# Kernel tuning notes

Measured on AMD Instinct MI355X. Metric: run time of the kernel, lower is better.

The kernel has to match this reference:

```python
import jax, jax.numpy as jnp
import numpy as np

N, E, H, L = 20000, 1_280_000, 64, 4


def setup_inputs() -> dict:
    key = jax.random.key(0)
    ks = jax.random.split(key, 24)
    inputs = jax.random.normal(ks[0], (1, N, 6), jnp.float32)
    node_masks = jnp.ones((1, N), jnp.int32)
    send_edges = jax.random.randint(ks[1], (E,), 0, N)
    recv_edges = jax.random.randint(ks[2], (E,), 0, N)

    def w(k, shape, scale=None):
        s = (1.0 / np.sqrt(shape[-2])) if scale is None else scale
        return (jax.random.normal(k, shape, jnp.float32) * s)

    d = dict(
        inputs=inputs, node_masks=node_masks,
        send_edges=send_edges, recv_edges=recv_edges,
        emb_w=w(ks[3], (1, H)), emb_b=jnp.zeros((H,), jnp.float32),
        edge_w1=w(ks[4], (L, 2 * H + 1, H)), edge_b1=jnp.zeros((L, H), jnp.float32),
        edge_w2=w(ks[5], (L, H, H)), edge_b2=jnp.zeros((L, H), jnp.float32),
        node_w1=w(ks[6], (L, 2 * H, H)), node_b1=jnp.zeros((L, H), jnp.float32),
        node_w2=w(ks[7], (L, H, H)), node_b2=jnp.zeros((L, H), jnp.float32),
        coord_w1=w(ks[8], (L, H, H)), coord_b1=jnp.zeros((L, H), jnp.float32),
        coord_wout=w(ks[9], (L, H, 1), scale=0.001),  # xavier gain=0.001, no bias
        vel_w1=w(ks[10], (L, H, H)), vel_b1=jnp.zeros((L, H), jnp.float32),
        vel_w2=w(ks[11], (L, H, 1)), vel_b2=jnp.zeros((L, 1), jnp.float32),
    )
    return d


def reference(inputs, node_masks, send_edges, recv_edges,
              emb_w, emb_b, edge_w1, edge_b1, edge_w2, edge_b2,
              node_w1, node_b1, node_w2, node_b2,
              coord_w1, coord_b1, coord_wout,
              vel_w1, vel_b1, vel_w2, vel_b2):
    silu = jax.nn.silu
    # node_masks is all-ones -> node_inds = arange(N); all nodes active.
    pos, vel = jnp.split(inputs, 2, axis=-1)          # [1,N,3] each
    h = jnp.linalg.norm(vel, axis=-1, keepdims=True)  # speed -> [1,N,1]
    h = h @ emb_w + emb_b                             # [1,N,H]
    coord = pos
    n = coord.shape[1]
    counts = jax.ops.segment_sum(jnp.ones_like(recv_edges, dtype=coord.dtype),
                                 recv_edges, num_segments=n)
    inv_cnt = (1.0 / jnp.maximum(counts, 1.0))[None, :, None]
    seg = lambda e: jax.ops.segment_sum(e, recv_edges, num_segments=n)

    for l in range(L):
        # coord2radial
        cd = coord[:, send_edges] - coord[:, recv_edges]        # [1,E,3]
        radial = jnp.sum(cd * cd, -1, keepdims=True)            # [1,E,1]
        # edge_model
        ef_in = jnp.concatenate([h[:, send_edges], h[:, recv_edges], radial], -1)
        ef = silu(silu(ef_in @ edge_w1[l] + edge_b1[l]) @ edge_w2[l] + edge_b2[l])
        # coord_model
        cm = silu(ef @ coord_w1[l] + coord_b1[l]) @ coord_wout[l]  # [1,E,1]
        trans = jnp.clip(cd * cm, -100.0, 100.0)
        agg_mean = jax.vmap(seg)(trans) * inv_cnt                  # scatter_mean
        # velocity update
        v_gate = silu(h @ vel_w1[l] + vel_b1[l]) @ vel_w2[l] + vel_b2[l]
        vel = agg_mean + v_gate * vel
        coord = coord + vel
        # node_model (recurrent residual)
        agg_sum = jax.vmap(seg)(ef)                                # scatter_sum
        hn = jnp.concatenate([h, agg_sum], -1)
        h = silu(hn @ node_w1[l] + node_b1[l]) @ node_w2[l] + node_b2[l] + h

    pred = jnp.concatenate([coord, vel], -1)  # [1,N,6] == pred_all (all active)
    return pred
```

## Files before the change

### kernel.cpp

```cpp
#include <hip/hip_runtime.h>
#include <math.h>

#define N_NODES 20000
#define N_EDGES 1280000
#define NLAYERS 4
#define NTILE (N_EDGES/32)
#define TSTRIDE 68
#define SCHUNK 79

typedef short bf16x8 __attribute__((ext_vector_type(8)));
typedef float f32x4  __attribute__((ext_vector_type(4)));
typedef long long i64;
typedef unsigned short us;

__device__ __forceinline__ float silu_f(float x) {
    return x / (1.0f + __expf(-x));
}

__device__ __forceinline__ us f2b(float x) {
    union { float f; unsigned u; } v; v.f = x;
    unsigned r = v.u + 0x7FFF + ((v.u >> 16) & 1);
    return (us)(r >> 16);
}
__device__ __forceinline__ float b2f(us u) {
    union { float f; unsigned u; } v; v.u = ((unsigned)u) << 16;
    return v.f;
}
__device__ __forceinline__ void split2r(float x, us& hi, us& lo) {
    hi = f2b(x);
    lo = f2b(x - b2f(hi));
}
__device__ __forceinline__ void split2f(float x, us& hi, us& lo) {
    union { float f; unsigned u; } v; v.f = x;
    hi = (us)(v.u >> 16);
    union { float f; unsigned u; } h; h.u = v.u & 0xFFFF0000u;
    union { float f; unsigned u; } r; r.f = x - h.f;
    lo = (us)(r.u >> 16);
}

__device__ __forceinline__ bf16x8 ld8(const us* p) {
    bf16x8 a;
    ((i64*)&a)[0] = *(const i64*)p;
    ((i64*)&a)[1] = *(const i64*)(p + 4);
    return a;
}

__device__ __forceinline__ void mfma3(f32x4& acc, bf16x8 ahi, bf16x8 alo,
                                      bf16x8 bhi, bf16x8 blo) {
    acc = __builtin_amdgcn_mfma_f32_16x16x32_bf16(ahi, bhi, acc, 0, 0, 0);
    acc = __builtin_amdgcn_mfma_f32_16x16x32_bf16(alo, bhi, acc, 0, 0, 0);
    acc = __builtin_amdgcn_mfma_f32_16x16x32_bf16(ahi, blo, acc, 0, 0, 0);
}

__global__ void k_init(const float* __restrict__ inp,
                       const float* __restrict__ emb_w,
                       const float* __restrict__ emb_b,
                       float* __restrict__ outv,
                       us* __restrict__ hbh, us* __restrict__ hbl) {
    int t = blockIdx.x * blockDim.x + threadIdx.x;
    int n = t >> 6, f = t & 63;
    if (n >= N_NODES) return;
    float vx = inp[n*6+3], vy = inp[n*6+4], vz = inp[n*6+5];
    float sp = sqrtf(vx*vx + vy*vy + vz*vz);
    float hv = sp * emb_w[f] + emb_b[f];
    us hi, lo; split2r(hv, hi, lo);
    hbh[t] = hi; hbl[t] = lo;
    if (f < 6) outv[n*6+f] = inp[n*6+f];
}

__global__ void k_cnt(const int* __restrict__ recv, int* __restrict__ counts) {
    int t = blockIdx.x*256 + threadIdx.x;
    if (t < N_EDGES) atomicAdd(&counts[recv[t]], 1);
}

__global__ void k_scan(const int* __restrict__ counts, int* __restrict__ rowstart,
                       int* __restrict__ cursor, int* __restrict__ tile2node) {
    __shared__ int buf[256];
    const int tid = threadIdx.x;
    const int lo = tid*SCHUNK;
    const int hi = (lo + SCHUNK < N_NODES) ? lo + SCHUNK : N_NODES;
    int s = 0;
    for (int i = lo; i < hi; ++i) s += counts[i];
    buf[tid] = s;
    __syncthreads();
    for (int off = 1; off < 256; off <<= 1) {
        int v = (tid >= off) ? buf[tid-off] : 0;
        __syncthreads();
        buf[tid] += v;
        __syncthreads();
    }
    int run = buf[tid] - s;
    for (int i = lo; i < hi; ++i) {
        rowstart[i] = run; cursor[i] = run;
        const int c = counts[i];
        for (int t = (run + 31) >> 5; t*32 < run + c; ++t) tile2node[t] = i;
        run += c;
    }
    if (tid < 20) rowstart[N_NODES + tid] = N_EDGES;
}

__global__ void k_scatter(const int* __restrict__ send, const int* __restrict__ recv,
                          int* __restrict__ cursor, us* __restrict__ sp16) {
    int t = blockIdx.x*256 + threadIdx.x;
    if (t < N_EDGES) {
        int p = atomicAdd(&cursor[recv[t]], 1);
        sp16[p] = (us)send[t];
    }
}

__global__ void k_prepw(const float* __restrict__ ew1, const float* __restrict__ ew2,
                        const float* __restrict__ cw1,
                        us* __restrict__ w1th, us* __restrict__ w1tl,
                        us* __restrict__ w2th, us* __restrict__ w2tl,
                        us* __restrict__ cw1th, us* __restrict__ cw1tl) {
    int t = blockIdx.x*256 + threadIdx.x;
    int l = t >> 14;
    int r = t & 16383;
    us hi, lo;
    if (r < 8192) {
        int n = r >> 7, k = r & 127;
        split2r(ew1[l*129*64 + k*64 + n], hi, lo);
        w1th[l*8192 + r] = hi; w1tl[l*8192 + r] = lo;
    } else if (r < 12288) {
        int rr = r - 8192; int n = rr >> 6, k = rr & 63;
        split2r(ew2[l*4096 + k*64 + n], hi, lo);
        w2th[l*4096 + n*64 + k] = hi; w2tl[l*4096 + n*64 + k] = lo;
    } else {
        int rr = r - 12288; int n = rr >> 6, k = rr & 63;
        split2r(cw1[l*4096 + k*64 + n], hi, lo);
        cw1th[l*4096 + n*64 + k] = hi; cw1tl[l*4096 + n*64 + k] = lo;
    }
}

__launch_bounds__(128, 4)
__global__ void k_edge(const us* __restrict__ sp16, const int* __restrict__ rowstart,
                       const int* __restrict__ tile2node,
                       const us* __restrict__ hbh, const us* __restrict__ hbl,
                       const float* __restrict__ outv,
                       const us* __restrict__ w1th, const us* __restrict__ w1tl,
                       const us* __restrict__ w2th, const us* __restrict__ w2tl,
                       const us* __restrict__ cw1th, const us* __restrict__ cw1tl,
                       const float* __restrict__ ew1, const float* __restrict__ eb1,
                       const float* __restrict__ eb2, const float* __restrict__ cb1,
                       const float* __restrict__ cwo,
                       float* __restrict__ aggs, float* __restrict__ aggm) {
    __shared__ us tileh[2][32*TSTRIDE];
    __shared__ us tilel[2][32*TSTRIDE];

    const int tid  = threadIdx.x;
    const int wid  = tid >> 6;
    const int lane = tid & 63;
    const int q    = lane >> 4;
    const int l15  = lane & 15;
    const int wbase = blockIdx.x*64 + wid*32;
    const int wtile = blockIdx.x*2 + wid;

    const int e0 = wbase + l15, e1 = e0 + 16;
    const int s0 = sp16[e0], s1 = sp16[e1];

    const int t2n = tile2node[wtile];
    const int wv = rowstart[t2n + 1 + l15];
    int seg0 = 0, seg1 = 0;
    #pragma unroll
    for (int i = 0; i < 16; ++i) {
        const int wi = __shfl(wv, i);
        seg0 += (e0 >= wi);
        seg1 += (e1 >= wi);
    }
    const int r0 = t2n + seg0, r1 = t2n + seg1;

    const float cdx0 = outv[s0*6+0]-outv[r0*6+0], cdy0 = outv[s0*6+1]-outv[r0*6+1], cdz0 = outv[s0*6+2]-outv[r0*6+2];
    const float cdx1 = outv[s1*6+0]-outv[r1*6+0], cdy1 = outv[s1*6+1]-outv[r1*6+1], cdz1 = outv[s1*6+2]-outv[r1*6+2];
    const float rad0 = cdx0*cdx0+cdy0*cdy0+cdz0*cdz0;
    const float rad1 = cdx1*cdx1+cdy1*cdy1+cdz1*cdz1;

    f32x4 acc[2][4];
    #pragma unroll
    for (int mu = 0; mu < 2; ++mu)
        #pragma unroll
        for (int t = 0; t < 4; ++t) acc[mu][t] = (f32x4){0.f,0.f,0.f,0.f};

    #pragma unroll
    for (int kc = 0; kc < 4; ++kc) {
        const int off = (kc & 1)*32 + q*8;
        const size_t o0 = (size_t)((kc < 2) ? s0 : r0)*64 + off;
        const size_t o1 = (size_t)((kc < 2) ? s1 : r1)*64 + off;
        bf16x8 a0h = ld8(hbh + o0), a0l = ld8(hbl + o0);
        bf16x8 a1h = ld8(hbh + o1), a1l = ld8(hbl + o1);
        #pragma unroll
        for (int t = 0; t < 4; ++t) {
            const int wo = (16*t + l15)*128 + kc*32 + q*8;
            bf16x8 bh = ld8(w1th + wo), bl = ld8(w1tl + wo);
            mfma3(acc[0][t], a0h, a0l, bh, bl);
            mfma3(acc[1][t], a1h, a1l, bh, bl);
        }
    }

    float rsh0[4], rsh1[4];
    #pragma unroll
    for (int r = 0; r < 4; ++r) {
        rsh0[r] = __shfl(rad0, 4*q + r);
        rsh1[r] = __shfl(rad1, 4*q + r);
    }
    #pragma unroll
    for (int t = 0; t < 4; ++t) {
        const int col = 16*t + l15;
        const float wl = ew1[128*64 + col];
        const float bb = eb1[col];
        #pragma unroll
        for (int r = 0; r < 4; ++r) {
            acc[0][t][r] += rsh0[r]*wl + bb;
            acc[1][t][r] += rsh1[r]*wl + bb;
        }
    }

    us* Th = tileh[wid];
    us* Tl = tilel[wid];
    #pragma unroll
    for (int mu = 0; mu < 2; ++mu)
        #pragma unroll
        for (int t = 0; t < 4; ++t)
            #pragma unroll
            for (int r = 0; r < 4; ++r) {
                us hi, lo; split2f(silu_f(acc[mu][t][r]), hi, lo);
                const int ti = (mu*16 + 4*q + r)*TSTRIDE + 16*t + l15;
                Th[ti] = hi; Tl[ti] = lo;
            }
    __asm__ volatile("s_waitcnt lgkmcnt(0)" ::: "memory");

    #pragma unroll
    for (int mu = 0; mu < 2; ++mu)
        #pragma unroll
        for (int t = 0; t < 4; ++t) acc[mu][t] = (f32x4){0.f,0.f,0.f,0.f};
    #pragma unroll
    for (int kc = 0; kc < 2; ++kc) {
        const int t0 = l15*TSTRIDE + kc*32 + q*8;
        const int t1i = (16+l15)*TSTRIDE + kc*32 + q*8;
        bf16x8 a0h = ld8(Th + t0),  a0l = ld8(Tl + t0);
        bf16x8 a1h = ld8(Th + t1i), a1l = ld8(Tl + t1i);
        #pragma unroll
        for (int t = 0; t < 4; ++t) {
            const int wo = (16*t + l15)*64 + kc*32 + q*8;
            bf16x8 bh = ld8(w2th + wo), bl = ld8(w2tl + wo);
            mfma3(acc[0][t], a0h, a0l, bh, bl);
            mfma3(acc[1][t], a1h, a1l, bh, bl);
        }
    }

    float ef[2][4][4];
    #pragma unroll
    for (int t = 0; t < 4; ++t) {
        const float bb = eb2[16*t + l15];
        #pragma unroll
        for (int mu = 0; mu < 2; ++mu)
            #pragma unroll
            for (int r = 0; r < 4; ++r)
                ef[mu][t][r] = silu_f(acc[mu][t][r] + bb);
    }
    __asm__ volatile("s_waitcnt lgkmcnt(0)" ::: "memory");
    #pragma unroll
    for (int mu = 0; mu < 2; ++mu)
        #pragma unroll
        for (int t = 0; t < 4; ++t)
            #pragma unroll
            for (int r = 0; r < 4; ++r) {
                us hi, lo; split2f(ef[mu][t][r], hi, lo);
                const int ti = (mu*16 + 4*q + r)*TSTRIDE + 16*t + l15;
                Th[ti] = hi; Tl[ti] = lo;
            }
    __asm__ volatile("s_waitcnt lgkmcnt(0)" ::: "memory");

    #pragma unroll
    for (int mu = 0; mu < 2; ++mu)
        #pragma unroll
        for (int t = 0; t < 4; ++t) acc[mu][t] = (f32x4){0.f,0.f,0.f,0.f};
    #pragma unroll
    for (int kc = 0; kc < 2; ++kc) {
        const int t0 = l15*TSTRIDE + kc*32 + q*8;
        const int t1i = (16+l15)*TSTRIDE + kc*32 + q*8;
        bf16x8 a0h = ld8(Th + t0),  a0l = ld8(Tl + t0);
        bf16x8 a1h = ld8(Th + t1i), a1l = ld8(Tl + t1i);
        #pragma unroll
        for (int t = 0; t < 4; ++t) {
            const int wo = (16*t + l15)*64 + kc*32 + q*8;
            bf16x8 bh = ld8(cw1th + wo), bl = ld8(cw1tl + wo);
            mfma3(acc[0][t], a0h, a0l, bh, bl);
            mfma3(acc[1][t], a1h, a1l, bh, bl);
        }
    }

    float cm0[4] = {0.f,0.f,0.f,0.f}, cm1[4] = {0.f,0.f,0.f,0.f};
    #pragma unroll
    for (int t = 0; t < 4; ++t) {
        const int col = 16*t + l15;
        const float cb = cb1[col];
        const float co = cwo[col];
        #pragma unroll
        for (int r = 0; r < 4; ++r) {
            cm0[r] += silu_f(acc[0][t][r] + cb) * co;
            cm1[r] += silu_f(acc[1][t][r] + cb) * co;
        }
    }
    #pragma unroll
    for (int m = 1; m <= 8; m <<= 1)
        #pragma unroll
        for (int r = 0; r < 4; ++r) {
            cm0[r] += __shfl_xor(cm0[r], m);
            cm1[r] += __shfl_xor(cm1[r], m);
        }

    int   sgrow[2][4];
    float tv[2][4];
    #pragma unroll
    for (int mu = 0; mu < 2; ++mu)
        #pragma unroll
        for (int r = 0; r < 4; ++r) {
            sgrow[mu][r] = __shfl(mu ? seg1 : seg0, 4*q + r);
            const float cxv = __shfl(mu ? cdx1 : cdx0, 4*q + r);
            const float cyv = __shfl(mu ? cdy1 : cdy0, 4*q + r);
            const float czv = __shfl(mu ? cdz1 : cdz0, 4*q + r);
            const float cmv = mu ? cm1[r] : cm0[r];
            const float sel = (l15 == 0) ? cxv : (l15 == 1) ? cyv : czv;
            tv[mu][r] = (l15 < 3) ? fminf(fmaxf(sel*cmv, -100.f), 100.f) : 0.f;
        }

    const int segA = __shfl(seg0, 0);
    const int segB = __shfl(seg1, 15);

    if (segB == segA) {
        float s4[4], trT = 0.f;
        #pragma unroll
        for (int t = 0; t < 4; ++t) {
            float v = 0.f;
            #pragma unroll
            for (int mu = 0; mu < 2; ++mu)
                #pragma unroll
                for (int r = 0; r < 4; ++r) v += ef[mu][t][r];
            v += __shfl_xor(v, 16);
            v += __shfl_xor(v, 32);
            s4[t] = v;
        }
        #pragma unroll
        for (int mu = 0; mu < 2; ++mu)
            #pragma unroll
            for (int r = 0; r < 4; ++r) trT += tv[mu][r];
        trT += __shfl_xor(trT, 16);
        trT += __shfl_xor(trT, 32);
        const int rn = t2n + segA;
        if (q == 0) {
            #pragma unroll
            for (int t = 0; t < 4; ++t)
                atomicAdd(&aggs[(size_t)rn*64 + 16*t + l15], s4[t]);
            if (l15 < 3) atomicAdd(&aggm[rn*3 + l15], trT);
        }
    } else if (segB == segA + 1) {
        float sA[4] = {0,0,0,0}, sB[4] = {0,0,0,0};
        float trA = 0.f, trB = 0.f;
        #pragma unroll
        for (int mu = 0; mu < 2; ++mu)
            #pragma unroll
            for (int r = 0; r < 4; ++r) {
                const bool isA = (sgrow[mu][r] == segA);
                #pragma unroll
                for (int t = 0; t < 4; ++t) {
                    const float v = ef[mu][t][r];
                    sA[t] += isA ? v : 0.f;
                    sB[t] += isA ? 0.f : v;
                }
                const float tvv = tv[mu][r];
                trA += isA ? tvv : 0.f;
                trB += isA ? 0.f : tvv;
            }
        #pragma unroll
        for (int t = 0; t < 4; ++t) {
            sA[t] += __shfl_xor(sA[t], 16); sA[t] += __shfl_xor(sA[t], 32);
            sB[t] += __shfl_xor(sB[t], 16); sB[t] += __shfl_xor(sB[t], 32);
        }
        trA += __shfl_xor(trA, 16); trA += __shfl_xor(trA, 32);
        trB += __shfl_xor(trB, 16); trB += __shfl_xor(trB, 32);
        const int rnA = t2n + segA, rnB = rnA + 1;
        if (q == 0) {
            #pragma unroll
            for (int t = 0; t < 4; ++t) {
                atomicAdd(&aggs[(size_t)rnA*64 + 16*t + l15], sA[t]);
                atomicAdd(&aggs[(size_t)rnB*64 + 16*t + l15], sB[t]);
            }
            if (l15 < 3) {
                atomicAdd(&aggm[rnA*3 + l15], trA);
                atomicAdd(&aggm[rnB*3 + l15], trB);
            }
        }
    } else {
        #pragma unroll
        for (int mu = 0; mu < 2; ++mu)
            #pragma unroll
            for (int r = 0; r < 4; ++r) {
                const int ren = t2n + sgrow[mu][r];
                #pragma unroll
                for (int t = 0; t < 4; ++t)
                    atomicAdd(&aggs[(size_t)ren*64 + 16*t + l15], ef[mu][t][r]);
                if (l15 < 3) atomicAdd(&aggm[ren*3 + l15], tv[mu][r]);
            }
    }
}

__launch_bounds__(256, 4)
__global__ void k_node(float* __restrict__ aggs, float* __restrict__ aggm,
                       const int* __restrict__ rowstart,
                       const float* __restrict__ VW1, const float* __restrict__ vb1,
                       const float* __restrict__ VW2, const float* __restrict__ vb2,
                       const float* __restrict__ NW1, const float* __restrict__ nb1,
                       const float* __restrict__ NW2, const float* __restrict__ nb2,
                       float* __restrict__ outv,
                       us* __restrict__ hbh, us* __restrict__ hbl) {
    __shared__ float hs[4][64], as[4][64], tt[4][64];
    const int tid = threadIdx.x;
    const int nn = tid >> 6, f = tid & 63;
    const int n = blockIdx.x*4 + nn;
    float hv = b2f(hbh[n*64+f]) + b2f(hbl[n*64+f]);
    hs[nn][f] = hv;
    as[nn][f] = aggs[n*64+f];
    aggs[n*64+f] = 0.f;
    __syncthreads();

    float a1 = vb1[f];
    for (int k = 0; k < 64; ++k) a1 += hs[nn][k] * VW1[k*64+f];
    float p = silu_f(a1) * VW2[f];
    #pragma unroll
    for (int o = 32; o > 0; o >>= 1) p += __shfl_down(p, o);
    float vgate = __shfl(p, 0) + vb2[0];

    if (f < 3) {
        float icnt = 1.0f / fmaxf((float)(rowstart[n+1] - rowstart[n]), 1.0f);
        float nv = aggm[n*3+f]*icnt + vgate*outv[n*6+3+f];
        aggm[n*3+f] = 0.f;
        outv[n*6+3+f] = nv;
        outv[n*6+f]  += nv;
    }

    float b = nb1[f];
    for (int k = 0; k < 64; ++k) b += hs[nn][k]*NW1[k*64+f];
    for (int k = 0; k < 64; ++k) b += as[nn][k]*NW1[(64+k)*64+f];
    __syncthreads();
    tt[nn][f] = silu_f(b);
    __syncthreads();
    float o = nb2[f] + hv;
    for (int k = 0; k < 64; ++k) o += tt[nn][k]*NW2[k*64+f];
    us hi, lo; split2r(o, hi, lo);
    hbh[n*64+f] = hi; hbl[n*64+f] = lo;
}

extern "C" void kernel_launch(void* const* d_in, const int* in_sizes, int n_in,
                              void* d_out, int out_size, void* d_ws, size_t ws_size,
                              hipStream_t stream) {
    const float* inp   = (const float*)d_in[0];
    const int*   send  = (const int*)d_in[2];
    const int*   recv  = (const int*)d_in[3];
    const float* emb_w = (const float*)d_in[4];
    const float* emb_b = (const float*)d_in[5];
    const float* ew1   = (const float*)d_in[6];
    const float* eb1   = (const float*)d_in[7];
    const float* ew2   = (const float*)d_in[8];
    const float* eb2   = (const float*)d_in[9];
    const float* nw1   = (const float*)d_in[10];
    const float* nb1   = (const float*)d_in[11];
    const float* nw2   = (const float*)d_in[12];
    const float* nb2   = (const float*)d_in[13];
    const float* cw1   = (const float*)d_in[14];
    const float* cb1   = (const float*)d_in[15];
    const float* cwo   = (const float*)d_in[16];
    const float* vw1   = (const float*)d_in[17];
    const float* vb1   = (const float*)d_in[18];
    const float* vw2   = (const float*)d_in[19];
    const float* vb2   = (const float*)d_in[20];

    float* outv = (float*)d_out;

    float* ws        = (float*)d_ws;
    float* aggs      = ws;
    float* aggm      = aggs + (size_t)N_NODES*64;
    int*   rowstart  = (int*)(aggm + N_NODES*3);
    int*   tile2node = rowstart + (N_NODES+20);
    us*    hbh       = (us*)(tile2node + NTILE);
    us*    hbl       = hbh + (size_t)N_NODES*64;
    us*    sp16      = hbl + (size_t)N_NODES*64;
    us*    w1th      = sp16 + N_EDGES;
    us*    w1tl      = w1th + 4*8192;
    us*    w2th      = w1tl + 4*8192;
    us*    w2tl      = w2th + 4*4096;
    us*    cw1th     = w2tl + 4*4096;
    us*    cw1tl     = cw1th + 4*4096;
    int*   counts    = (int*)aggs;
    int*   cursor    = counts + N_NODES;

    hipMemsetAsync(counts, 0, N_NODES*sizeof(int), stream);
    k_init<<<(N_NODES*64)/256, 256, 0, stream>>>(inp, emb_w, emb_b, outv, hbh, hbl);
    k_cnt<<<(N_EDGES+255)/256, 256, 0, stream>>>(recv, counts);
    k_scan<<<1, 256, 0, stream>>>(counts, rowstart, cursor, tile2node);
    k_scatter<<<(N_EDGES+255)/256, 256, 0, stream>>>(send, recv, cursor, sp16);
    k_prepw<<<256, 256, 0, stream>>>(ew1, ew2, cw1, w1th, w1tl, w2th, w2tl, cw1th, cw1tl);
    hipMemsetAsync(aggs, 0, (size_t)N_NODES*67*sizeof(float), stream);

    for (int l = 0; l < NLAYERS; ++l) {
        k_edge<<<N_EDGES/64, 128, 0, stream>>>(sp16, rowstart, tile2node, hbh, hbl, outv,
            w1th + l*8192, w1tl + l*8192,
            w2th + l*4096, w2tl + l*4096,
            cw1th + l*4096, cw1tl + l*4096,
            ew1 + (size_t)l*129*64, eb1 + l*64, eb2 + l*64,
            cb1 + l*64, cwo + l*64,
            aggs, aggm);
        k_node<<<N_NODES/4, 256, 0, stream>>>(aggs, aggm, rowstart,
            vw1 + (size_t)l*64*64, vb1 + l*64, vw2 + l*64, vb2 + l,
            nw1 + (size_t)l*128*64, nb1 + l*64,
            nw2 + (size_t)l*64*64,  nb2 + l*64,
            outv, hbh, hbl);
    }
}
```

Measured before the change: 2.047 ms.

## Make edge kernel persistent with software prefetch of next tile's indices and features

```diff
diff --git a/kernel.cpp b/kernel.cpp
--- a/kernel.cpp
+++ b/kernel.cpp
@@ -5,6 +5,7 @@
 #define N_EDGES 1280000
 #define NLAYERS 4
 #define NTILE (N_EDGES/32)
+#define NWAVES 4096
 #define TSTRIDE 68
 #define SCHUNK 79
 
@@ -152,255 +153,306 @@
     const int lane = tid & 63;
     const int q    = lane >> 4;
     const int l15  = lane & 15;
-    const int wbase = blockIdx.x*64 + wid*32;
-    const int wtile = blockIdx.x*2 + wid;
-
-    const int e0 = wbase + l15, e1 = e0 + 16;
-    const int s0 = sp16[e0], s1 = sp16[e1];
-
-    const int t2n = tile2node[wtile];
-    const int wv = rowstart[t2n + 1 + l15];
-    int seg0 = 0, seg1 = 0;
-    #pragma unroll
-    for (int i = 0; i < 16; ++i) {
-        const int wi = __shfl(wv, i);
-        seg0 += (e0 >= wi);
-        seg1 += (e1 >= wi);
-    }
-    const int r0 = t2n + seg0, r1 = t2n + seg1;
-
-    const float cdx0 = outv[s0*6+0]-outv[r0*6+0], cdy0 = outv[s0*6+1]-outv[r0*6+1], cdz0 = outv[s0*6+2]-outv[r0*6+2];
-    const float cdx1 = outv[s1*6+0]-outv[r1*6+0], cdy1 = outv[s1*6+1]-outv[r1*6+1], cdz1 = outv[s1*6+2]-outv[r1*6+2];
-    const float rad0 = cdx0*cdx0+cdy0*cdy0+cdz0*cdz0;
-    const float rad1 = cdx1*cdx1+cdy1*cdy1+cdz1*cdz1;
-
-    f32x4 acc[2][4];
-    #pragma unroll
-    for (int mu = 0; mu < 2; ++mu)
-        #pragma unroll
-        for (int t = 0; t < 4; ++t) acc[mu][t] = (f32x4){0.f,0.f,0.f,0.f};
-
-    #pragma unroll
-    for (int kc = 0; kc < 4; ++kc) {
-        const int off = (kc & 1)*32 + q*8;
-        const size_t o0 = (size_t)((kc < 2) ? s0 : r0)*64 + off;
-        const size_t o1 = (size_t)((kc < 2) ? s1 : r1)*64 + off;
-        bf16x8 a0h = ld8(hbh + o0), a0l = ld8(hbl + o0);
-        bf16x8 a1h = ld8(hbh + o1), a1l = ld8(hbl + o1);
-        #pragma unroll
-        for (int t = 0; t < 4; ++t) {
-            const int wo = (16*t + l15)*128 + kc*32 + q*8;
-            bf16x8 bh = ld8(w1th + wo), bl = ld8(w1tl + wo);
-            mfma3(acc[0][t], a0h, a0l, bh, bl);
-            mfma3(acc[1][t], a1h, a1l, bh, bl);
-        }
-    }
-
-    float rsh0[4], rsh1[4];
-    #pragma unroll
-    for (int r = 0; r < 4; ++r) {
-        rsh0[r] = __shfl(rad0, 4*q + r);
-        rsh1[r] = __shfl(rad1, 4*q + r);
-    }
-    #pragma unroll
-    for (int t = 0; t < 4; ++t) {
-        const int col = 16*t + l15;
-        const float wl = ew1[128*64 + col];
-        const float bb = eb1[col];
-        #pragma unroll
-        for (int r = 0; r < 4; ++r) {
-            acc[0][t][r] += rsh0[r]*wl + bb;
-            acc[1][t][r] += rsh1[r]*wl + bb;
-        }
-    }
+    const int q8   = q*8;
 
     us* Th = tileh[wid];
     us* Tl = tilel[wid];
-    #pragma unroll
-    for (int mu = 0; mu < 2; ++mu)
-        #pragma unroll
-        for (int t = 0; t < 4; ++t)
+
+    int tile = blockIdx.x*2 + wid;
+    if (tile >= NTILE) return;
+
+    int p_s0  = sp16[tile*32 + l15];
+    int p_s1  = sp16[tile*32 + 16 + l15];
+    int p_t2n = tile2node[tile];
+    int p_wv  = rowstart[p_t2n + 1 + l15];
+    bf16x8 g0h = ld8(hbh + (size_t)p_s0*64 + q8);
+    bf16x8 g0l = ld8(hbl + (size_t)p_s0*64 + q8);
+    bf16x8 g1h = ld8(hbh + (size_t)p_s1*64 + q8);
+    bf16x8 g1l = ld8(hbl + (size_t)p_s1*64 + q8);
+
+    while (true) {
+        const int s0 = p_s0, s1 = p_s1, t2n = p_t2n, wv = p_wv;
+        const int e0 = tile*32 + l15, e1 = e0 + 16;
+
+        int seg0 = 0, seg1 = 0;
+        #pragma unroll
+        for (int i = 0; i < 16; ++i) {
+            const int wi = __shfl(wv, i);
+            seg0 += (e0 >= wi);
+            seg1 += (e1 >= wi);
+        }
+        const int r0 = t2n + seg0, r1 = t2n + seg1;
+
+        const float cdx0 = outv[s0*6+0]-outv[r0*6+0], cdy0 = outv[s0*6+1]-outv[r0*6+1], cdz0 = outv[s0*6+2]-outv[r0*6+2];
+        const float cdx1 = outv[s1*6+0]-outv[r1*6+0], cdy1 = outv[s1*6+1]-outv[r1*6+1], cdz1 = outv[s1*6+2]-outv[r1*6+2];
+        const float rad0 = cdx0*cdx0+cdy0*cdy0+cdz0*cdz0;
+        const float rad1 = cdx1*cdx1+cdy1*cdy1+cdz1*cdz1;
+
+        bf16x8 s0h1 = ld8(hbh + (size_t)s0*64 + 32 + q8), s0l1 = ld8(hbl + (size_t)s0*64 + 32 + q8);
+        bf16x8 s1h1 = ld8(hbh + (size_t)s1*64 + 32 + q8), s1l1 = ld8(hbl + (size_t)s1*64 + 32 + q8);
+        bf16x8 r0h0 = ld8(hbh + (size_t)r0*64 + q8),      r0l0 = ld8(hbl + (size_t)r0*64 + q8);
+        bf16x8 r0h1 = ld8(hbh + (size_t)r0*64 + 32 + q8), r0l1 = ld8(hbl + (size_t)r0*64 + 32 + q8);
+        bf16x8 r1h0 = ld8(hbh + (size_t)r1*64 + q8),      r1l0 = ld8(hbl + (size_t)r1*64 + q8);
+        bf16x8 r1h1 = ld8(hbh + (size_t)r1*64 + 32 + q8), r1l1 = ld8(hbl + (size_t)r1*64 + 32 + q8);
+
+        f32x4 acc[2][4];
+        #pragma unroll
+        for (int mu = 0; mu < 2; ++mu)
+            #pragma unroll
+            for (int t = 0; t < 4; ++t) acc[mu][t] = (f32x4){0.f,0.f,0.f,0.f};
+
+        #pragma unroll
+        for (int t = 0; t < 4; ++t) {
+            const int wo = (16*t + l15)*128 + q8;
+            bf16x8 bh = ld8(w1th + wo), bl = ld8(w1tl + wo);
+            mfma3(acc[0][t], g0h, g0l, bh, bl);
+            mfma3(acc[1][t], g1h, g1l, bh, bl);
+        }
+        #pragma unroll
+        for (int t = 0; t < 4; ++t) {
+            const int wo = (16*t + l15)*128 + 32 + q8;
+            bf16x8 bh = ld8(w1th + wo), bl = ld8(w1tl + wo);
+            mfma3(acc[0][t], s0h1, s0l1, bh, bl);
+            mfma3(acc[1][t], s1h1, s1l1, bh, bl);
+        }
+        #pragma unroll
+        for (int t = 0; t < 4; ++t) {
+            const int wo = (16*t + l15)*128 + 64 + q8;
+            bf16x8 bh = ld8(w1th + wo), bl = ld8(w1tl + wo);
+            mfma3(acc[0][t], r0h0, r0l0, bh, bl);
+            mfma3(acc[1][t], r1h0, r1l0, bh, bl);
+        }
+        #pragma unroll
+        for (int t = 0; t < 4; ++t) {
+            const int wo = (16*t + l15)*128 + 96 + q8;
+            bf16x8 bh = ld8(w1th + wo), bl = ld8(w1tl + wo);
+            mfma3(acc[0][t], r0h1, r0l1, bh, bl);
+            mfma3(acc[1][t], r1h1, r1l1, bh, bl);
+        }
+
+        const int ntile = tile + NWAVES;
+        if (ntile < NTILE) {
+            p_s0  = sp16[ntile*32 + l15];
+            p_s1  = sp16[ntile*32 + 16 + l15];
+            p_t2n = tile2node[ntile];
+        }
+
+        float rsh0[4], rsh1[4];
+        #pragma unroll
+        for (int r = 0; r < 4; ++r) {
+            rsh0[r] = __shfl(rad0, 4*q + r);
+            rsh1[r] = __shfl(rad1, 4*q + r);
+        }
+        #pragma unroll
+        for (int t = 0; t < 4; ++t) {
+            const int col = 16*t + l15;
+            const float wl = ew1[128*64 + col];
+            const float bb = eb1[col];
             #pragma unroll
             for (int r = 0; r < 4; ++r) {
-                us hi, lo; split2f(silu_f(acc[mu][t][r]), hi, lo);
-                const int ti = (mu*16 + 4*q + r)*TSTRIDE + 16*t + l15;
-                Th[ti] = hi; Tl[ti] = lo;
-            }
-    __asm__ volatile("s_waitcnt lgkmcnt(0)" ::: "memory");
-
-    #pragma unroll
-    for (int mu = 0; mu < 2; ++mu)
-        #pragma unroll
-        for (int t = 0; t < 4; ++t) acc[mu][t] = (f32x4){0.f,0.f,0.f,0.f};
-    #pragma unroll
-    for (int kc = 0; kc < 2; ++kc) {
-        const int t0 = l15*TSTRIDE + kc*32 + q*8;
-        const int t1i = (16+l15)*TSTRIDE + kc*32 + q*8;
-        bf16x8 a0h = ld8(Th + t0),  a0l = ld8(Tl + t0);
-        bf16x8 a1h = ld8(Th + t1i), a1l = ld8(Tl + t1i);
-        #pragma unroll
-        for (int t = 0; t < 4; ++t) {
-            const int wo = (16*t + l15)*64 + kc*32 + q*8;
-            bf16x8 bh = ld8(w2th + wo), bl = ld8(w2tl + wo);
-            mfma3(acc[0][t], a0h, a0l, bh, bl);
-            mfma3(acc[1][t], a1h, a1l, bh, bl);
-        }
-    }
-
-    float ef[2][4][4];
-    #pragma unroll
-    for (int t = 0; t < 4; ++t) {
-        const float bb = eb2[16*t + l15];
+                acc[0][t][r] += rsh0[r]*wl + bb;
+                acc[1][t][r] += rsh1[r]*wl + bb;
+            }
+        }
+
+        __asm__ volatile("s_waitcnt lgkmcnt(0)" ::: "memory");
         #pragma unroll
         for (int mu = 0; mu < 2; ++mu)
             #pragma unroll
-            for (int r = 0; r < 4; ++r)
-                ef[mu][t][r] = silu_f(acc[mu][t][r] + bb);
-    }
-    __asm__ volatile("s_waitcnt lgkmcnt(0)" ::: "memory");
-    #pragma unroll
-    for (int mu = 0; mu < 2; ++mu)
-        #pragma unroll
-        for (int t = 0; t < 4; ++t)
+            for (int t = 0; t < 4; ++t)
+                #pragma unroll
+                for (int r = 0; r < 4; ++r) {
+                    us hi, lo; split2f(silu_f(acc[mu][t][r]), hi, lo);
+                    const int ti = (mu*16 + 4*q + r)*TSTRIDE + 16*t + l15;
+                    Th[ti] = hi; Tl[ti] = lo;
+                }
+        __asm__ volatile("s_waitcnt lgkmcnt(0)" ::: "memory");
+
+        #pragma unroll
+        for (int mu = 0; mu < 2; ++mu)
+            #pragma unroll
+            for (int t = 0; t < 4; ++t) acc[mu][t] = (f32x4){0.f,0.f,0.f,0.f};
+        #pragma unroll
+        for (int kc = 0; kc < 2; ++kc) {
+            const int t0 = l15*TSTRIDE + kc*32 + q8;
+            const int t1i = (16+l15)*TSTRIDE + kc*32 + q8;
+            bf16x8 a0h = ld8(Th + t0),  a0l = ld8(Tl + t0);
+            bf16x8 a1h = ld8(Th + t1i), a1l = ld8(Tl + t1i);
+            #pragma unroll
+            for (int t = 0; t < 4; ++t) {
+                const int wo = (16*t + l15)*64 + kc*32 + q8;
+                bf16x8 bh = ld8(w2th + wo), bl = ld8(w2tl + wo);
+                mfma3(acc[0][t], a0h, a0l, bh, bl);
+                mfma3(acc[1][t], a1h, a1l, bh, bl);
+            }
+        }
+
+        if (ntile < NTILE) {
+            p_wv = rowstart[p_t2n + 1 + l15];
+            g0h = ld8(hbh + (size_t)p_s0*64 + q8);
+            g0l = ld8(hbl + (size_t)p_s0*64 + q8);
+            g1h = ld8(hbh + (size_t)p_s1*64 + q8);
+            g1l = ld8(hbl + (size_t)p_s1*64 + q8);
+        }
+
+        float ef[2][4][4];
+        #pragma unroll
+        for (int t = 0; t < 4; ++t) {
+            const float bb = eb2[16*t + l15];
+            #pragma unroll
+            for (int mu = 0; mu < 2; ++mu)
+                #pragma unroll
+                for (int r = 0; r < 4; ++r)
+                    ef[mu][t][r] = silu_f(acc[mu][t][r] + bb);
+        }
+        __asm__ volatile("s_waitcnt lgkmcnt(0)" ::: "memory");
+        #pragma unroll
+        for (int mu = 0; mu < 2; ++mu)
+            #pragma unroll
+            for (int t = 0; t < 4; ++t)
+                #pragma unroll
+                for (int r = 0; r < 4; ++r) {
+                    us hi, lo; split2f(ef[mu][t][r], hi, lo);
+                    const int ti = (mu*16 + 4*q + r)*TSTRIDE + 16*t + l15;
+                    Th[ti] = hi; Tl[ti] = lo;
+                }
+        __asm__ volatile("s_waitcnt lgkmcnt(0)" ::: "memory");
+
+        #pragma unroll
+        for (int mu = 0; mu < 2; ++mu)
+            #pragma unroll
+            for (int t = 0; t < 4; ++t) acc[mu][t] = (f32x4){0.f,0.f,0.f,0.f};
+        #pragma unroll
+        for (int kc = 0; kc < 2; ++kc) {
+            const int t0 = l15*TSTRIDE + kc*32 + q8;
+            const int t1i = (16+l15)*TSTRIDE + kc*32 + q8;
+            bf16x8 a0h = ld8(Th + t0),  a0l = ld8(Tl + t0);
+            bf16x8 a1h = ld8(Th + t1i), a1l = ld8(Tl + t1i);
+            #pragma unroll
+            for (int t = 0; t < 4; ++t) {
+                const int wo = (16*t + l15)*64 + kc*32 + q8;
+                bf16x8 bh = ld8(cw1th + wo), bl = ld8(cw1tl + wo);
+                mfma3(acc[0][t], a0h, a0l, bh, bl);
+                mfma3(acc[1][t], a1h, a1l, bh, bl);
+            }
+        }
+
+        float cm0[4] = {0.f,0.f,0.f,0.f}, cm1[4] = {0.f,0.f,0.f,0.f};
+        #pragma unroll
+        for (int t = 0; t < 4; ++t) {
+            const int col = 16*t + l15;
+            const float cb = cb1[col];
+            const float co = cwo[col];
             #pragma unroll
             for (int r = 0; r < 4; ++r) {
-                us hi, lo; split2f(ef[mu][t][r], hi, lo);
-                const int ti = (mu*16 + 4*q + r)*TSTRIDE + 16*t + l15;
-                Th[ti] = hi; Tl[ti] = lo;
-            }
-    __asm__ volatile("s_waitcnt lgkmcnt(0)" ::: "memory");
-
-    #pragma unroll
-    for (int mu = 0; mu < 2; ++mu)
-        #pragma unroll
-        for (int t = 0; t < 4; ++t) acc[mu][t] = (f32x4){0.f,0.f,0.f,0.f};
-    #pragma unroll
-    for (int kc = 0; kc < 2; ++kc) {
-        const int t0 = l15*TSTRIDE + kc*32 + q*8;
-        const int t1i = (16+l15)*TSTRIDE + kc*32 + q*8;
-        bf16x8 a0h = ld8(Th + t0),  a0l = ld8(Tl + t0);
-        bf16x8 a1h = ld8(Th + t1i), a1l = ld8(Tl + t1i);
-        #pragma unroll
-        for (int t = 0; t < 4; ++t) {
-            const int wo = (16*t + l15)*64 + kc*32 + q*8;
-            bf16x8 bh = ld8(cw1th + wo), bl = ld8(cw1tl + wo);
-            mfma3(acc[0][t], a0h, a0l, bh, bl);
-            mfma3(acc[1][t], a1h, a1l, bh, bl);
-        }
-    }
-
-    float cm0[4] = {0.f,0.f,0.f,0.f}, cm1[4] = {0.f,0.f,0.f,0.f};
-    #pragma unroll
-    for (int t = 0; t < 4; ++t) {
-        const int col = 16*t + l15;
-        const float cb = cb1[col];
-        const float co = cwo[col];
-        #pragma unroll
-        for (int r = 0; r < 4; ++r) {
-            cm0[r] += silu_f(acc[0][t][r] + cb) * co;
-            cm1[r] += silu_f(acc[1][t][r] + cb) * co;
-        }
-    }
-    #pragma unroll
-    for (int m = 1; m <= 8; m <<= 1)
-        #pragma unroll
-        for (int r = 0; r < 4; ++r) {
-            cm0[r] += __shfl_xor(cm0[r], m);
-            cm1[r] += __shfl_xor(cm1[r], m);
-        }
-
-    int   sgrow[2][4];
-    float tv[2][4];
-    #pragma unroll
-    for (int mu = 0; mu < 2; ++mu)
-        #pragma unroll
-        for (int r = 0; r < 4; ++r) {
-            sgrow[mu][r] = __shfl(mu ? seg1 : seg0, 4*q + r);
-            const float cxv = __shfl(mu ? cdx1 : cdx0, 4*q + r);
-            const float cyv = __shfl(mu ? cdy1 : cdy0, 4*q + r);
-            const float czv = __shfl(mu ? cdz1 : cdz0, 4*q + r);
-            const float cmv = mu ? cm1[r] : cm0[r];
-            const float sel = (l15 == 0) ? cxv : (l15 == 1) ? cyv : czv;
-            tv[mu][r] = (l15 < 3) ? fminf(fmaxf(sel*cmv, -100.f), 100.f) : 0.f;
-        }
-
-    const int segA = __shfl(seg0, 0);
-    const int segB = __shfl(seg1, 15);
-
-    if (segB == segA) {
-        float s4[4], trT = 0.f;
-        #pragma unroll
-        for (int t = 0; t < 4; ++t) {
-            float v = 0.f;
+                cm0[r] += silu_f(acc[0][t][r] + cb) * co;
+                cm1[r] += silu_f(acc[1][t][r] + cb) * co;
+            }
+        }
+        #pragma unroll
+        for (int m = 1; m <= 8; m <<= 1)
+            #pragma unroll
+            for (int r = 0; r < 4; ++r) {
+                cm0[r] += __shfl_xor(cm0[r], m);
+                cm1[r] += __shfl_xor(cm1[r], m);
+            }
+
+        int   sgrow[2][4];
+        float tv[2][4];
+        #pragma unroll
+        for (int mu = 0; mu < 2; ++mu)
+            #pragma unroll
+            for (int r = 0; r < 4; ++r) {
+                sgrow[mu][r] = __shfl(mu ? seg1 : seg0, 4*q + r);
+                const float cxv = __shfl(mu ? cdx1 : cdx0, 4*q + r);
+                const float cyv = __shfl(mu ? cdy1 : cdy0, 4*q + r);
+                const float czv = __shfl(mu ? cdz1 : cdz0, 4*q + r);
+                const float cmv = mu ? cm1[r] : cm0[r];
+                const float sel = (l15 == 0) ? cxv : (l15 == 1) ? cyv : czv;
+                tv[mu][r] = (l15 < 3) ? fminf(fmaxf(sel*cmv, -100.f), 100.f) : 0.f;
+            }
+
+        const int segA = __shfl(seg0, 0);
+        const int segB = __shfl(seg1, 15);
+
+        if (segB == segA) {
+            float s4[4], trT = 0.f;
+            #pragma unroll
+            for (int t = 0; t < 4; ++t) {
+                float v = 0.f;
+                #pragma unroll
+                for (int mu = 0; mu < 2; ++mu)
+                    #pragma unroll
+                    for (int r = 0; r < 4; ++r) v += ef[mu][t][r];
+                v += __shfl_xor(v, 16);
+                v += __shfl_xor(v, 32);
+                s4[t] = v;
+            }
             #pragma unroll
             for (int mu = 0; mu < 2; ++mu)
                 #pragma unroll
-                for (int r = 0; r < 4; ++r) v += ef[mu][t][r];
-            v += __shfl_xor(v, 16);
-            v += __shfl_xor(v, 32);
-            s4[t] = v;
-        }
-        #pragma unroll
-        for (int mu = 0; mu < 2; ++mu)
-            #pragma unroll
-            for (int r = 0; r < 4; ++r) trT += tv[mu][r];
-        trT += __shfl_xor(trT, 16);
-        trT += __shfl_xor(trT, 32);
-        const int rn = t2n + segA;
-        if (q == 0) {
-            #pragma unroll
-            for (int t = 0; t < 4; ++t)
-                atomicAdd(&aggs[(size_t)rn*64 + 16*t + l15], s4[t]);
-            if (l15 < 3) atomicAdd(&aggm[rn*3 + l15], trT);
-        }
-    } else if (segB == segA + 1) {
-        float sA[4] = {0,0,0,0}, sB[4] = {0,0,0,0};
-        float trA = 0.f, trB = 0.f;
-        #pragma unroll
-        for (int mu = 0; mu < 2; ++mu)
-            #pragma unroll
-            for (int r = 0; r < 4; ++r) {
-                const bool isA = (sgrow[mu][r] == segA);
+                for (int r = 0; r < 4; ++r) trT += tv[mu][r];
+            trT += __shfl_xor(trT, 16);
+            trT += __shfl_xor(trT, 32);
+            const int rn = t2n + segA;
+            if (q == 0) {
+                #pragma unroll
+                for (int t = 0; t < 4; ++t)
+                    atomicAdd(&aggs[(size_t)rn*64 + 16*t + l15], s4[t]);
+                if (l15 < 3) atomicAdd(&aggm[rn*3 + l15], trT);
+            }
+        } else if (segB == segA + 1) {
+            float sA[4] = {0,0,0,0}, sB[4] = {0,0,0,0};
+            float trA = 0.f, trB = 0.f;
+            #pragma unroll
+            for (int mu = 0; mu < 2; ++mu)
+                #pragma unroll
+                for (int r = 0; r < 4; ++r) {
+                    const bool isA = (sgrow[mu][r] == segA);
+                    #pragma unroll
+                    for (int t = 0; t < 4; ++t) {
+                        const float v = ef[mu][t][r];
+                        sA[t] += isA ? v : 0.f;
+                        sB[t] += isA ? 0.f : v;
+                    }
+                    const float tvv = tv[mu][r];
+                    trA += isA ? tvv : 0.f;
+                    trB += isA ? 0.f : tvv;
+                }
+            #pragma unroll
+            for (int t = 0; t < 4; ++t) {
+                sA[t] += __shfl_xor(sA[t], 16); sA[t] += __shfl_xor(sA[t], 32);
+                sB[t] += __shfl_xor(sB[t], 16); sB[t] += __shfl_xor(sB[t], 32);
+            }
+            trA += __shfl_xor(trA, 16); trA += __shfl_xor(trA, 32);
+            trB += __shfl_xor(trB, 16); trB += __shfl_xor(trB, 32);
+            const int rnA = t2n + segA, rnB = rnA + 1;
+            if (q == 0) {
                 #pragma unroll
                 for (int t = 0; t < 4; ++t) {
-                    const float v = ef[mu][t][r];
-                    sA[t] += isA ? v : 0.f;
-                    sB[t] += isA ? 0.f : v;
+                    atomicAdd(&aggs[(size_t)rnA*64 + 16*t + l15], sA[t]);
+                    atomicAdd(&aggs[(size_t)rnB*64 + 16*t + l15], sB[t]);
                 }
-                const float tvv = tv[mu][r];
-                trA += isA ? tvv : 0.f;
-                trB += isA ? 0.f : tvv;
-            }
-        #pragma unroll
-        for (int t = 0; t < 4; ++t) {
-            sA[t] += __shfl_xor(sA[t], 16); sA[t] += __shfl_xor(sA[t], 32);
-            sB[t] += __shfl_xor(sB[t], 16); sB[t] += __shfl_xor(sB[t], 32);
-        }
-        trA += __shfl_xor(trA, 16); trA += __shfl_xor(trA, 32);
-        trB += __shfl_xor(trB, 16); trB += __shfl_xor(trB, 32);
-        const int rnA = t2n + segA, rnB = rnA + 1;
-        if (q == 0) {
-            #pragma unroll
-            for (int t = 0; t < 4; ++t) {
-                atomicAdd(&aggs[(size_t)rnA*64 + 16*t + l15], sA[t]);
-                atomicAdd(&aggs[(size_t)rnB*64 + 16*t + l15], sB[t]);
-            }
-            if (l15 < 3) {
-                atomicAdd(&aggm[rnA*3 + l15], trA);
-                atomicAdd(&aggm[rnB*3 + l15], trB);
-            }
-        }
-    } else {
-        #pragma unroll
-        for (int mu = 0; mu < 2; ++mu)
-            #pragma unroll
-            for (int r = 0; r < 4; ++r) {
-                const int ren = t2n + sgrow[mu][r];
-                #pragma unroll
-                for (int t = 0; t < 4; ++t)
-                    atomicAdd(&aggs[(size_t)ren*64 + 16*t + l15], ef[mu][t][r]);
-                if (l15 < 3) atomicAdd(&aggm[ren*3 + l15], tv[mu][r]);
-            }
+                if (l15 < 3) {
+                    atomicAdd(&aggm[rnA*3 + l15], trA);
+                    atomicAdd(&aggm[rnB*3 + l15], trB);
+                }
+            }
+        } else {
+            #pragma unroll
+            for (int mu = 0; mu < 2; ++mu)
+                #pragma unroll
+                for (int r = 0; r < 4; ++r) {
+                    const int ren = t2n + sgrow[mu][r];
+                    #pragma unroll
+                    for (int t = 0; t < 4; ++t)
+                        atomicAdd(&aggs[(size_t)ren*64 + 16*t + l15], ef[mu][t][r]);
+                    if (l15 < 3) atomicAdd(&aggm[ren*3 + l15], tv[mu][r]);
+                }
+        }
+
+        if (ntile >= NTILE) break;
+        tile = ntile;
     }
 }
 
@@ -502,7 +554,7 @@
     hipMemsetAsync(aggs, 0, (size_t)N_NODES*67*sizeof(float), stream);
 
     for (int l = 0; l < NLAYERS; ++l) {
-        k_edge<<<N_EDGES/64, 128, 0, stream>>>(sp16, rowstart, tile2node, hbh, hbl, outv,
+        k_edge<<<NWAVES/2, 128, 0, stream>>>(sp16, rowstart, tile2node, hbh, hbl, outv,
             w1th + l*8192, w1tl + l*8192,
             w2th + l*4096, w2tl + l*4096,
             cw1th + l*4096, cw1tl + l*4096,
```

Measured after the change: 3.361 ms. 1.64x slower.

## Precompute per-node receiver projection of edge MLP first layer

Applied to the files above, without the earlier changes.

```diff
diff --git a/kernel.cpp b/kernel.cpp
--- a/kernel.cpp
+++ b/kernel.cpp
@@ -132,15 +132,32 @@
     }
 }
 
+__launch_bounds__(256, 4)
+__global__ void k_recv(const us* __restrict__ hbh, const us* __restrict__ hbl,
+                       const float* __restrict__ ew1,
+                       const float* __restrict__ eb1,
+                       float* __restrict__ R) {
+    __shared__ float hs[4][64];
+    const int tid = threadIdx.x;
+    const int nn = tid >> 6, f = tid & 63;
+    const int n = blockIdx.x*4 + nn;
+    hs[nn][f] = b2f(hbh[(size_t)n*64+f]) + b2f(hbl[(size_t)n*64+f]);
+    __syncthreads();
+    float s = eb1[f];
+    for (int k = 0; k < 64; ++k) s += hs[nn][k] * ew1[(64+k)*64 + f];
+    R[(size_t)n*64+f] = s;
+}
+
 __launch_bounds__(128, 4)
 __global__ void k_edge(const us* __restrict__ sp16, const int* __restrict__ rowstart,
                        const int* __restrict__ tile2node,
                        const us* __restrict__ hbh, const us* __restrict__ hbl,
                        const float* __restrict__ outv,
+                       const float* __restrict__ R,
                        const us* __restrict__ w1th, const us* __restrict__ w1tl,
                        const us* __restrict__ w2th, const us* __restrict__ w2tl,
                        const us* __restrict__ cw1th, const us* __restrict__ cw1tl,
-                       const float* __restrict__ ew1, const float* __restrict__ eb1,
+                       const float* __restrict__ ew1,
                        const float* __restrict__ eb2, const float* __restrict__ cb1,
                        const float* __restrict__ cwo,
                        float* __restrict__ aggs, float* __restrict__ aggm) {
@@ -169,27 +186,54 @@
     }
     const int r0 = t2n + seg0, r1 = t2n + seg1;
 
+    int sgrow[2][4];
+    #pragma unroll
+    for (int r = 0; r < 4; ++r) {
+        sgrow[0][r] = __shfl(seg0, 4*q + r);
+        sgrow[1][r] = __shfl(seg1, 4*q + r);
+    }
+    const int segA = __shfl(seg0, 0);
+    const int segB = __shfl(seg1, 15);
+
     const float cdx0 = outv[s0*6+0]-outv[r0*6+0], cdy0 = outv[s0*6+1]-outv[r0*6+1], cdz0 = outv[s0*6+2]-outv[r0*6+2];
     const float cdx1 = outv[s1*6+0]-outv[r1*6+0], cdy1 = outv[s1*6+1]-outv[r1*6+1], cdz1 = outv[s1*6+2]-outv[r1*6+2];
     const float rad0 = cdx0*cdx0+cdy0*cdy0+cdz0*cdz0;
     const float rad1 = cdx1*cdx1+cdy1*cdy1+cdz1*cdz1;
 
     f32x4 acc[2][4];
-    #pragma unroll
-    for (int mu = 0; mu < 2; ++mu)
-        #pragma unroll
-        for (int t = 0; t < 4; ++t) acc[mu][t] = (f32x4){0.f,0.f,0.f,0.f};
-
-    #pragma unroll
-    for (int kc = 0; kc < 4; ++kc) {
-        const int off = (kc & 1)*32 + q*8;
-        const size_t o0 = (size_t)((kc < 2) ? s0 : r0)*64 + off;
-        const size_t o1 = (size_t)((kc < 2) ? s1 : r1)*64 + off;
+
+    if (segB == segA) {
+        const int rn = t2n + segA;
+        #pragma unroll
+        for (int t = 0; t < 4; ++t) {
+            const float rv = R[(size_t)rn*64 + 16*t + l15];
+            #pragma unroll
+            for (int mu = 0; mu < 2; ++mu)
+                #pragma unroll
+                for (int r = 0; r < 4; ++r) acc[mu][t][r] = rv;
+        }
+    } else {
+        #pragma unroll
+        for (int mu = 0; mu < 2; ++mu)
+            #pragma unroll
+            for (int r = 0; r < 4; ++r) {
+                const size_t ro = (size_t)(t2n + sgrow[mu][r])*64;
+                #pragma unroll
+                for (int t = 0; t < 4; ++t)
+                    acc[mu][t][r] = R[ro + 16*t + l15];
+            }
+    }
+
+    #pragma unroll
+    for (int kc = 0; kc < 2; ++kc) {
+        const int off = kc*32 + q*8;
+        const size_t o0 = (size_t)s0*64 + off;
+        const size_t o1 = (size_t)s1*64 + off;
         bf16x8 a0h = ld8(hbh + o0), a0l = ld8(hbl + o0);
         bf16x8 a1h = ld8(hbh + o1), a1l = ld8(hbl + o1);
         #pragma unroll
         for (int t = 0; t < 4; ++t) {
-            const int wo = (16*t + l15)*128 + kc*32 + q*8;
+            const int wo = (16*t + l15)*128 + off;
             bf16x8 bh = ld8(w1th + wo), bl = ld8(w1tl + wo);
             mfma3(acc[0][t], a0h, a0l, bh, bl);
             mfma3(acc[1][t], a1h, a1l, bh, bl);
@@ -204,13 +248,11 @@
     }
     #pragma unroll
     for (int t = 0; t < 4; ++t) {
-        const int col = 16*t + l15;
-        const float wl = ew1[128*64 + col];
-        const float bb = eb1[col];
+        const float wl = ew1[128*64 + 16*t + l15];
         #pragma unroll
         for (int r = 0; r < 4; ++r) {
-            acc[0][t][r] += rsh0[r]*wl + bb;
-            acc[1][t][r] += rsh1[r]*wl + bb;
+            acc[0][t][r] += rsh0[r]*wl;
+            acc[1][t][r] += rsh1[r]*wl;
         }
     }
 
@@ -309,13 +351,11 @@
             cm1[r] += __shfl_xor(cm1[r], m);
         }
 
-    int   sgrow[2][4];
     float tv[2][4];
     #pragma unroll
     for (int mu = 0; mu < 2; ++mu)
         #pragma unroll
         for (int r = 0; r < 4; ++r) {
-            sgrow[mu][r] = __shfl(mu ? seg1 : seg0, 4*q + r);
             const float cxv = __shfl(mu ? cdx1 : cdx0, 4*q + r);
             const float cyv = __shfl(mu ? cdy1 : cdy0, 4*q + r);
             const float czv = __shfl(mu ? cdz1 : cdz0, 4*q + r);
@@ -323,9 +363,6 @@
             const float sel = (l15 == 0) ? cxv : (l15 == 1) ? cyv : czv;
             tv[mu][r] = (l15 < 3) ? fminf(fmaxf(sel*cmv, -100.f), 100.f) : 0.f;
         }
-
-    const int segA = __shfl(seg0, 0);
-    const int segB = __shfl(seg1, 15);
 
     if (segB == segA) {
         float s4[4], trT = 0.f;
@@ -490,6 +527,7 @@
     us*    w2tl      = w2th + 4*4096;
     us*    cw1th     = w2tl + 4*4096;
     us*    cw1tl     = cw1th + 4*4096;
+    float* R         = (float*)(cw1tl + 4*4096);
     int*   counts    = (int*)aggs;
     int*   cursor    = counts + N_NODES;
 
@@ -502,11 +540,13 @@
     hipMemsetAsync(aggs, 0, (size_t)N_NODES*67*sizeof(float), stream);
 
     for (int l = 0; l < NLAYERS; ++l) {
-        k_edge<<<N_EDGES/64, 128, 0, stream>>>(sp16, rowstart, tile2node, hbh, hbl, outv,
+        k_recv<<<N_NODES/4, 256, 0, stream>>>(hbh, hbl,
+            ew1 + (size_t)l*129*64, eb1 + l*64, R);
+        k_edge<<<N_EDGES/64, 128, 0, stream>>>(sp16, rowstart, tile2node, hbh, hbl, outv, R,
             w1th + l*8192, w1tl + l*8192,
             w2th + l*4096, w2tl + l*4096,
             cw1th + l*4096, cw1tl + l*4096,
-            ew1 + (size_t)l*129*64, eb1 + l*64, eb2 + l*64,
+            ew1 + (size_t)l*129*64, eb2 + l*64,
             cb1 + l*64, cwo + l*64,
             aggs, aggm);
         k_node<<<N_NODES/4, 256, 0, stream>>>(aggs, aggm, rowstart,
```

New measurement: 1.845 ms. 9.9% less time.
